# Kernel optimization log

Hardware: AMD Instinct MI355X
Metric: run time of the kernel (lower is better)

The kernel has to match this reference:

```python
import jax, jax.numpy as jnp
import numpy as np
import math

TAU = 2.0
EPS = 1e-5
ALPHA = 2.0  # spikingjelly surrogate.ATan default alpha

@jax.custom_vjp
def atan_spike(x):
    return (x >= 0.0).astype(x.dtype)

def _spike_fwd(x):
    return atan_spike(x), x

def _spike_bwd(x, g):
    s = math.pi / 2.0 * ALPHA
    return (g * (ALPHA / 2.0) / (1.0 + (s * x) ** 2),)

atan_spike.defvjp(_spike_fwd, _spike_bwd)

def lif_seq(x_seq):
    # MultiStepLIFNode: v' = v + (x - v)/tau ; spike = H(v'-1) ; hard reset to v_reset=0
    def step(v, x):
        v = v + (x - v) / TAU
        s = atan_spike(v - 1.0)
        v = v * (1.0 - jax.lax.stop_gradient(s))  # detach_reset=True
        return v, s
    _, s_seq = jax.lax.scan(step, jnp.zeros_like(x_seq[0]), x_seq)
    return s_seq

def setup_inputs() -> dict:
    key = jax.random.key(0)
    kx, kw = jax.random.split(key)
    T, B, N, P, D = 4, 64, 1024, 63, 128
    x = jax.random.normal(kx, (T, B, N, P), dtype=jnp.float32)
    W = jax.random.normal(kw, (D, P), dtype=jnp.float32) * np.float32(1.0 / np.sqrt(P))
    gamma = jnp.ones((D,), dtype=jnp.float32)
    beta = jnp.zeros((D,), dtype=jnp.float32)
    return {"x": x, "W": W, "gamma": gamma, "beta": beta, "pe": 0}

def reference(x, W, gamma, beta, pe):
    # bias-free Linear: [T,B,N,P] x [D,P] -> [T,B,N,D]
    h = jnp.einsum('tbnp,dp->tbnd', x, W)
    # BatchNorm1d over channel D; training-mode batch stats over (T*B, N)
    mean = jnp.mean(h, axis=(0, 1, 2), keepdims=True)
    var = jnp.var(h, axis=(0, 1, 2), keepdims=True)  # biased, as torch BN normalization
    h = (h - mean) * jax.lax.rsqrt(var + EPS) * gamma + beta
    # multi-step LIF across T (self.pe=False -> tAPE branch skipped)
    out = lif_seq(h)  # [T,B,N,D] == original output after final transpose
    return out
```

## Files before the change

kernel.cpp:

```cpp
#include <hip/hip_runtime.h>
#include <math.h>

#define T_STEPS 4
#define R_ROWS  65536
#define M_ROWS  262144
#define P_DIM   63
#define D_DIM   128
#define PP      64

#define TILES_TOTAL (M_ROWS / 64)
#define G_CHUNKS 8

__global__ __launch_bounds__(256) void gram_kernel(const float* __restrict__ x,
                                                   double* __restrict__ partials,
                                                   int tiles_per_block) {
    __shared__ __align__(16) float xt[2][64 * PP];
    const int tid = threadIdx.x;
    const int tj = tid & 15;
    const int ti = tid >> 4;

    double dacc[4][4];
#pragma unroll
    for (int a = 0; a < 4; a++)
#pragma unroll
        for (int b = 0; b < 4; b++) dacc[a][b] = 0.0;

    if (tid < 64) {
        xt[0][tid * PP + 63] = 1.0f;
        xt[1][tid * PP + 63] = 1.0f;
    }

    const int tile0 = blockIdx.x * tiles_per_block;
    float4 reg[4];

    {
        const float4* src = (const float4*)(x + (size_t)tile0 * (64 * 63));
#pragma unroll
        for (int it = 0; it < 4; it++) {
            int k = tid + it * 256;
            reg[it] = (k < 1008) ? src[k] : make_float4(0.f, 0.f, 0.f, 0.f);
        }
    }
#pragma unroll
    for (int it = 0; it < 4; it++) {
        int k = tid + it * 256;
        if (k < 1008) {
            const float* ve = (const float*)&reg[it];
            int flat = k * 4;
#pragma unroll
            for (int e = 0; e < 4; e++) {
                int f = flat + e;
                int r = f / 63;
                int c = f - r * 63;
                xt[0][r * PP + c] = ve[e];
            }
        }
    }
    __syncthreads();

    for (int t = 0; t < tiles_per_block; t++) {
        const int cur = t & 1;
        if (t + 1 < tiles_per_block) {
            const float4* src = (const float4*)(x + (size_t)(tile0 + t + 1) * (64 * 63));
#pragma unroll
            for (int it = 0; it < 4; it++) {
                int k = tid + it * 256;
                reg[it] = (k < 1008) ? src[k] : make_float4(0.f, 0.f, 0.f, 0.f);
            }
        }

        float facc[4][4];
#pragma unroll
        for (int a = 0; a < 4; a++)
#pragma unroll
            for (int b = 0; b < 4; b++) facc[a][b] = 0.0f;

        const float* buf = xt[cur];
        for (int r = 0; r < 64; r++) {
            float4 xi = *(const float4*)&buf[r * PP + ti * 4];
            float4 xj = *(const float4*)&buf[r * PP + tj * 4];
            const float* xia = (const float*)&xi;
            const float* xja = (const float*)&xj;
#pragma unroll
            for (int a = 0; a < 4; a++)
#pragma unroll
                for (int b = 0; b < 4; b++)
                    facc[a][b] = fmaf(xia[a], xja[b], facc[a][b]);
        }
#pragma unroll
        for (int a = 0; a < 4; a++)
#pragma unroll
            for (int b = 0; b < 4; b++) dacc[a][b] += (double)facc[a][b];

        __syncthreads();
        if (t + 1 < tiles_per_block) {
            float* nbuf = xt[1 - cur];
#pragma unroll
            for (int it = 0; it < 4; it++) {
                int k = tid + it * 256;
                if (k < 1008) {
                    const float* ve = (const float*)&reg[it];
                    int flat = k * 4;
#pragma unroll
                    for (int e = 0; e < 4; e++) {
                        int f = flat + e;
                        int r = f / 63;
                        int c = f - r * 63;
                        nbuf[r * PP + c] = ve[e];
                    }
                }
            }
            __syncthreads();
        }
    }

    double* Pb = partials + (size_t)blockIdx.x * 4096;
#pragma unroll
    for (int a = 0; a < 4; a++)
#pragma unroll
        for (int b = 0; b < 4; b++)
            Pb[(ti * 4 + a) * 64 + (tj * 4 + b)] = dacc[a][b];
}

__global__ __launch_bounds__(256) void reduce_kernel(const double* __restrict__ partials,
                                                     double* __restrict__ G8,
                                                     int copies_per_chunk) {
    const int chunk = blockIdx.x >> 4;
    const int idx   = (blockIdx.x & 15) * 256 + threadIdx.x;
    const double* src = partials + (size_t)chunk * copies_per_chunk * 4096;
    double s = 0.0;
    for (int c = 0; c < copies_per_chunk; c++)
        s += src[(size_t)c * 4096 + idx];
    G8[(size_t)chunk * 4096 + idx] = s;
}

__global__ __launch_bounds__(64) void stats_kernel(const double* __restrict__ G,
                                                   const float* __restrict__ W,
                                                   const float* __restrict__ gamma,
                                                   const float* __restrict__ beta,
                                                   float* __restrict__ stats) {
    const int d = blockIdx.x;
    const int p = threadIdx.x;
    __shared__ float sW[64];
    sW[p] = (p < P_DIM) ? W[d * P_DIM + p] : 0.0f;
    __syncthreads();

    double inner = 0.0;
#pragma unroll
    for (int c = 0; c < G_CHUNKS; c++) {
        const double* Gr = G + (size_t)c * (64 * 64) + p * 64;
        for (int q = 0; q < 64; q++) inner += Gr[q] * (double)sW[q];
    }

    double contrib = (double)sW[p] * inner;
    double ex2M = contrib;
#pragma unroll
    for (int off = 32; off > 0; off >>= 1) ex2M += __shfl_down(ex2M, off, 64);
    double meanM = __shfl(inner, 63, 64);

    if (p == 0) {
        double mean = meanM / (double)M_ROWS;
        double ex2  = ex2M  / (double)M_ROWS;
        double var  = ex2 - mean * mean;
        float varf  = (float)var;
        float vpe   = varf + 1e-5f;
        float invstd = (float)(1.0 / sqrt((double)vpe));
        stats[d * 4 + 0] = (float)mean;
        stats[d * 4 + 1] = invstd;
        stats[d * 4 + 2] = gamma[d];
        stats[d * 4 + 3] = beta[d];
    }
}

#define LIF_ROWS 32
__global__ __launch_bounds__(256, 2) void lif_kernel(const float* __restrict__ x,
                                                     const float* __restrict__ W,
                                                     const float* __restrict__ stats,
                                                     float* __restrict__ out) {
    __shared__ __align__(16) float sw[P_DIM * D_DIM];
    __shared__ __align__(16) float sx[T_STEPS * LIF_ROWS * 64];
    const int tid = threadIdx.x;

    for (int k = tid; k < P_DIM * D_DIM; k += 256) sx[k] = W[k];
    __syncthreads();
    for (int k = tid; k < P_DIM * D_DIM; k += 256) {
        int p = k >> 7;
        int d = k & 127;
        sw[k] = sx[d * P_DIM + p];
    }
    __syncthreads();

    const int r0 = blockIdx.x * LIF_ROWS;
    const int seg = tid >> 6;
    const int lane = tid & 63;
    const float4* src = (const float4*)(x + ((size_t)seg * R_ROWS + r0) * P_DIM);
    for (int k = lane; k < 504; k += 64) {
        float4 v = src[k];
        const float* ve = (const float*)&v;
        int flat = k * 4;
#pragma unroll
        for (int e = 0; e < 4; e++) {
            int f = flat + e;
            int r = f / 63;
            int c = f - r * 63;
            int cs = (((c >> 2) ^ ((r >> 1) & 3)) << 2) | (c & 3);
            sx[(seg * LIF_ROWS + r) * 64 + cs] = ve[e];
        }
    }
    __syncthreads();

    const int td = tid & 15;
    const int tr = tid >> 4;
    const int d0 = td * 8;
    const int lr0 = tr * 2;
    const int sq0 = (lr0 >> 1) & 3;

    float acc[T_STEPS][2][8];
#pragma unroll
    for (int t = 0; t < T_STEPS; t++)
#pragma unroll
        for (int i = 0; i < 2; i++)
#pragma unroll
            for (int j = 0; j < 8; j++) acc[t][i][j] = 0.0f;

    for (int pq = 0; pq < 15; pq++) {
        const int p0 = pq * 4;
        float4 w[4][2];
#pragma unroll
        for (int pp = 0; pp < 4; pp++)
#pragma unroll
            for (int h = 0; h < 2; h++)
                w[pp][h] = *(const float4*)&sw[(p0 + pp) * D_DIM + d0 + h * 4];

        const int xq = (pq ^ sq0) << 2;
#pragma unroll
        for (int t = 0; t < T_STEPS; t++)
#pragma unroll
            for (int i = 0; i < 2; i++) {
                float4 xv = *(const float4*)&sx[(t * LIF_ROWS + lr0 + i) * 64 + xq];
                const float xe[4] = {xv.x, xv.y, xv.z, xv.w};
                float* a = acc[t][i];
#pragma unroll
                for (int pp = 0; pp < 4; pp++) {
#pragma unroll
                    for (int h = 0; h < 2; h++) {
                        const float4 ww = w[pp][h];
                        a[h * 4 + 0] = fmaf(xe[pp], ww.x, a[h * 4 + 0]);
                        a[h * 4 + 1] = fmaf(xe[pp], ww.y, a[h * 4 + 1]);
                        a[h * 4 + 2] = fmaf(xe[pp], ww.z, a[h * 4 + 2]);
                        a[h * 4 + 3] = fmaf(xe[pp], ww.w, a[h * 4 + 3]);
                    }
                }
            }
    }

#pragma unroll
    for (int p = 60; p < 63; p++) {
        float4 wA = *(const float4*)&sw[p * D_DIM + d0];
        float4 wB = *(const float4*)&sw[p * D_DIM + d0 + 4];
        const int cs = ((15 ^ sq0) << 2) | (p & 3);
#pragma unroll
        for (int t = 0; t < T_STEPS; t++)
#pragma unroll
            for (int i = 0; i < 2; i++) {
                float xv = sx[(t * LIF_ROWS + lr0 + i) * 64 + cs];
                float* a = acc[t][i];
                a[0] = fmaf(xv, wA.x, a[0]);
                a[1] = fmaf(xv, wA.y, a[1]);
                a[2] = fmaf(xv, wA.z, a[2]);
                a[3] = fmaf(xv, wA.w, a[3]);
                a[4] = fmaf(xv, wB.x, a[4]);
                a[5] = fmaf(xv, wB.y, a[5]);
                a[6] = fmaf(xv, wB.z, a[6]);
                a[7] = fmaf(xv, wB.w, a[7]);
            }
    }

#pragma unroll
    for (int i = 0; i < 2; i++) {
        const int row = r0 + lr0 + i;
        float sval[T_STEPS][8];
#pragma unroll
        for (int j = 0; j < 8; j++) {
            float4 st = ((const float4*)stats)[d0 + j];
            float v = 0.0f;
#pragma unroll
            for (int t = 0; t < T_STEPS; t++) {
                float hn = (acc[t][i][j] - st.x) * st.y;
                hn = hn * st.z;
                hn = hn + st.w;
                v = v + (hn - v) * 0.5f;
                float s = (v >= 1.0f) ? 1.0f : 0.0f;
                sval[t][j] = s;
                if (s != 0.0f) v = 0.0f;
            }
        }
#pragma unroll
        for (int t = 0; t < T_STEPS; t++) {
            float* ob = &out[((size_t)t * R_ROWS + row) * D_DIM + d0];
            *(float4*)ob       = make_float4(sval[t][0], sval[t][1], sval[t][2], sval[t][3]);
            *(float4*)(ob + 4) = make_float4(sval[t][4], sval[t][5], sval[t][6], sval[t][7]);
        }
    }
}

extern "C" void kernel_launch(void* const* d_in, const int* in_sizes, int n_in,
                              void* d_out, int out_size, void* d_ws, size_t ws_size,
                              hipStream_t stream) {
    const float* x     = (const float*)d_in[0];
    const float* W     = (const float*)d_in[1];
    const float* gamma = (const float*)d_in[2];
    const float* beta  = (const float*)d_in[3];
    float* out = (float*)d_out;

    const size_t fixed = (size_t)G_CHUNKS * 4096 * 8 + 4096;
    int nparts = 512;
    while (nparts > 64 && (size_t)nparts * 4096 * 8 + fixed > ws_size) nparts >>= 1;
    const int tiles_per_block = TILES_TOTAL / nparts;

    double* partials = (double*)d_ws;
    double* G8       = (double*)((char*)d_ws + (size_t)nparts * 4096 * 8);
    float*  stats    = (float*)((char*)G8 + (size_t)G_CHUNKS * 4096 * 8);

    gram_kernel<<<nparts, 256, 0, stream>>>(x, partials, tiles_per_block);
    reduce_kernel<<<G_CHUNKS * 16, 256, 0, stream>>>(partials, G8, nparts / G_CHUNKS);
    stats_kernel<<<D_DIM, 64, 0, stream>>>(G8, W, gamma, beta, stats);
    lif_kernel<<<R_ROWS / LIF_ROWS, 256, 0, stream>>>(x, W, stats, out);
}
```

Before: 291.7 us.

## Pretranspose W globally and halve LIF shared-memory weight tile for higher occupancy

Adds a small kernel that writes the transposed weight matrix to workspace once, so each LIF block loads it straight with float4 copies instead of staging and transposing it in shared memory. The shared weight tile is cut to 32 rows: the second half is prefetched into registers and swapped into shared memory between the two halves of the P loop. Launch bounds go from 2 to 3 blocks per CU so more blocks can be resident. The cost is an extra launch, more register pressure from the prefetch buffers, and an added barrier pair.

```diff
diff --git a/kernel.cpp b/kernel.cpp
--- a/kernel.cpp
+++ b/kernel.cpp
@@ -10,6 +10,16 @@
 
 #define TILES_TOTAL (M_ROWS / 64)
 #define G_CHUNKS 8
+
+__global__ __launch_bounds__(256) void wt_kernel(const float* __restrict__ W,
+                                                 float* __restrict__ Wt) {
+    int j = blockIdx.x * 256 + threadIdx.x;
+    if (j < P_DIM * D_DIM) {
+        int p = j >> 7;
+        int d = j & 127;
+        Wt[j] = W[d * P_DIM + p];
+    }
+}
 
 __global__ __launch_bounds__(256) void gram_kernel(const float* __restrict__ x,
                                                    double* __restrict__ partials,
@@ -173,22 +183,26 @@
 }
 
 #define LIF_ROWS 32
-__global__ __launch_bounds__(256, 2) void lif_kernel(const float* __restrict__ x,
-                                                     const float* __restrict__ W,
+__global__ __launch_bounds__(256, 3) void lif_kernel(const float* __restrict__ x,
+                                                     const float* __restrict__ Wt,
                                                      const float* __restrict__ stats,
                                                      float* __restrict__ out) {
-    __shared__ __align__(16) float sw[P_DIM * D_DIM];
+    __shared__ __align__(16) float sw[32 * D_DIM];
     __shared__ __align__(16) float sx[T_STEPS * LIF_ROWS * 64];
     const int tid = threadIdx.x;
 
-    for (int k = tid; k < P_DIM * D_DIM; k += 256) sx[k] = W[k];
-    __syncthreads();
-    for (int k = tid; k < P_DIM * D_DIM; k += 256) {
-        int p = k >> 7;
-        int d = k & 127;
-        sw[k] = sx[d * P_DIM + p];
-    }
-    __syncthreads();
+    const float4* wt4 = (const float4*)Wt;
+#pragma unroll
+    for (int i = 0; i < 4; i++) {
+        int k = tid + i * 256;
+        ((float4*)sw)[k] = wt4[k];
+    }
+    float4 h1[4];
+#pragma unroll
+    for (int i = 0; i < 4; i++) {
+        int k = tid + i * 256;
+        h1[i] = (k < 992) ? wt4[1024 + k] : make_float4(0.f, 0.f, 0.f, 0.f);
+    }
 
     const int r0 = blockIdx.x * LIF_ROWS;
     const int seg = tid >> 6;
@@ -223,7 +237,7 @@
 #pragma unroll
             for (int j = 0; j < 8; j++) acc[t][i][j] = 0.0f;
 
-    for (int pq = 0; pq < 15; pq++) {
+    for (int pq = 0; pq < 8; pq++) {
         const int p0 = pq * 4;
         float4 w[4][2];
 #pragma unroll
@@ -241,7 +255,7 @@
                 const float xe[4] = {xv.x, xv.y, xv.z, xv.w};
                 float* a = acc[t][i];
 #pragma unroll
-                for (int pp = 0; pp < 4; pp++) {
+                for (int pp = 0; pp < 4; pp++)
 #pragma unroll
                     for (int h = 0; h < 2; h++) {
                         const float4 ww = w[pp][h];
@@ -250,14 +264,52 @@
                         a[h * 4 + 2] = fmaf(xe[pp], ww.z, a[h * 4 + 2]);
                         a[h * 4 + 3] = fmaf(xe[pp], ww.w, a[h * 4 + 3]);
                     }
-                }
+            }
+    }
+
+    __syncthreads();
+#pragma unroll
+    for (int i = 0; i < 4; i++) {
+        int k = tid + i * 256;
+        if (k < 992) ((float4*)sw)[k] = h1[i];
+    }
+    __syncthreads();
+
+    for (int pq = 8; pq < 15; pq++) {
+        const int lp0 = pq * 4 - 32;
+        float4 w[4][2];
+#pragma unroll
+        for (int pp = 0; pp < 4; pp++)
+#pragma unroll
+            for (int h = 0; h < 2; h++)
+                w[pp][h] = *(const float4*)&sw[(lp0 + pp) * D_DIM + d0 + h * 4];
+
+        const int xq = (pq ^ sq0) << 2;
+#pragma unroll
+        for (int t = 0; t < T_STEPS; t++)
+#pragma unroll
+            for (int i = 0; i < 2; i++) {
+                float4 xv = *(const float4*)&sx[(t * LIF_ROWS + lr0 + i) * 64 + xq];
+                const float xe[4] = {xv.x, xv.y, xv.z, xv.w};
+                float* a = acc[t][i];
+#pragma unroll
+                for (int pp = 0; pp < 4; pp++)
+#pragma unroll
+                    for (int h = 0; h < 2; h++) {
+                        const float4 ww = w[pp][h];
+                        a[h * 4 + 0] = fmaf(xe[pp], ww.x, a[h * 4 + 0]);
+                        a[h * 4 + 1] = fmaf(xe[pp], ww.y, a[h * 4 + 1]);
+                        a[h * 4 + 2] = fmaf(xe[pp], ww.z, a[h * 4 + 2]);
+                        a[h * 4 + 3] = fmaf(xe[pp], ww.w, a[h * 4 + 3]);
+                    }
             }
     }
 
 #pragma unroll
     for (int p = 60; p < 63; p++) {
-        float4 wA = *(const float4*)&sw[p * D_DIM + d0];
-        float4 wB = *(const float4*)&sw[p * D_DIM + d0 + 4];
+        const int lp = p - 32;
+        float4 wA = *(const float4*)&sw[lp * D_DIM + d0];
+        float4 wB = *(const float4*)&sw[lp * D_DIM + d0 + 4];
         const int cs = ((15 ^ sq0) << 2) | (p & 3);
 #pragma unroll
         for (int t = 0; t < T_STEPS; t++)
@@ -313,7 +365,7 @@
     const float* beta  = (const float*)d_in[3];
     float* out = (float*)d_out;
 
-    const size_t fixed = (size_t)G_CHUNKS * 4096 * 8 + 4096;
+    const size_t fixed = (size_t)G_CHUNKS * 4096 * 8 + 2048 + 32768 + 4096;
     int nparts = 512;
     while (nparts > 64 && (size_t)nparts * 4096 * 8 + fixed > ws_size) nparts >>= 1;
     const int tiles_per_block = TILES_TOTAL / nparts;
@@ -321,9 +373,11 @@
     double* partials = (double*)d_ws;
     double* G8       = (double*)((char*)d_ws + (size_t)nparts * 4096 * 8);
     float*  stats    = (float*)((char*)G8 + (size_t)G_CHUNKS * 4096 * 8);
-
+    float*  Wt       = (float*)((char*)stats + 2048);
+
+    wt_kernel<<<(P_DIM * D_DIM + 255) / 256, 256, 0, stream>>>(W, Wt);
     gram_kernel<<<nparts, 256, 0, stream>>>(x, partials, tiles_per_block);
     reduce_kernel<<<G_CHUNKS * 16, 256, 0, stream>>>(partials, G8, nparts / G_CHUNKS);
     stats_kernel<<<D_DIM, 64, 0, stream>>>(G8, W, gamma, beta, stats);
-    lif_kernel<<<R_ROWS / LIF_ROWS, 256, 0, stream>>>(x, W, stats, out);
-}
+    lif_kernel<<<R_ROWS / LIF_ROWS, 256, 0, stream>>>(x, Wt, stats, out);
+}
```

Result: slower. 298.1 us (+2.2%).
